# Kernel optimization log

Measured on AMD Instinct MI355X. Metric: run time of the kernel, lower is better.

## Reference

```python
import jax, jax.numpy as jnp
import numpy as np

B, S, T, H, E, V = 64, 128, 64, 512, 256, 10000


def setup_inputs() -> dict:
    key = jax.random.key(0)
    ks = jax.random.split(key, 16)
    w = 0.05
    return {
        "trg": jax.random.randint(ks[0], (B, T), 0, V),
        "encoder_hidden": jax.random.normal(ks[1], (B, S, 2 * H), jnp.float32),
        "src_lengths": jax.random.randint(ks[2], (B,), 1, S + 1),
        "h0": jax.random.normal(ks[3], (B, H), jnp.float32),
        "c0": jax.random.normal(ks[4], (B, H), jnp.float32),
        "emb_table": jax.random.normal(ks[5], (V, E), jnp.float32) * w,
        "Wkey": jax.random.normal(ks[6], (2 * H, H), jnp.float32) * w,      # attention.key_layer
        "Wquery": jax.random.normal(ks[7], (H, H), jnp.float32) * w,        # attention.query_layer
        "we": jax.random.normal(ks[8], (H,), jnp.float32) * w,              # attention.energy_layer
        "W_ih": jax.random.normal(ks[9], (4 * H, E + 2 * H), jnp.float32) * w,
        "W_hh": jax.random.normal(ks[10], (4 * H, H), jnp.float32) * w,
        "b_ih": jnp.zeros((4 * H,), jnp.float32),
        "b_hh": jnp.zeros((4 * H,), jnp.float32),
        "Wpre": jax.random.normal(ks[11], (3 * H + E, H), jnp.float32) * w,  # pre_output_layer (no bias)
        "Wgen": jax.random.normal(ks[12], (H, V), jnp.float32) * w,          # generator / softmax head
    }


def reference(trg, encoder_hidden, src_lengths, h0, c0, emb_table, Wkey, Wquery,
              we, W_ih, W_hh, b_ih, b_hh, Wpre, Wgen):
    # Teacher-forced unroll (teacher_forcing=True branch); dropout in eval mode.
    s = encoder_hidden.shape[1]
    proj_key = encoder_hidden @ Wkey                            # [B,S,H]
    mask = jnp.arange(s)[None, :] < src_lengths[:, None]        # [B,S]
    embs = emb_table[trg]                                       # [B,T,E]

    def step(carry, emb_t):
        h, c = carry                                            # [B,H] each
        q = h @ Wquery                                          # query = last-layer hidden
        e = jnp.einsum('bsh,h->bs', jnp.tanh(q[:, None, :] + proj_key), we)
        a = jax.nn.softmax(jnp.where(mask, e, -1e9), axis=-1)   # masked attention
        ctx = jnp.einsum('bs,bsd->bd', a, encoder_hidden)       # [B,2H]
        x = jnp.concatenate([emb_t, ctx], axis=-1)              # rnn_input
        g = x @ W_ih.T + h @ W_hh.T + b_ih + b_hh
        i_g, f_g, g_g, o_g = jnp.split(g, 4, axis=-1)           # torch LSTM gate order
        c_new = jax.nn.sigmoid(f_g) * c + jax.nn.sigmoid(i_g) * jnp.tanh(g_g)
        h_new = jax.nn.sigmoid(o_g) * jnp.tanh(c_new)
        pre = jnp.concatenate([emb_t, h_new, ctx], axis=-1) @ Wpre
        logp = jax.nn.log_softmax(pre @ Wgen, axis=-1)          # [B,V]
        return (h_new, c_new), logp

    (hf, cf), out = jax.lax.scan(step, (h0, c0), jnp.swapaxes(embs, 0, 1))
    return jnp.transpose(out, (1, 2, 0)), hf, cf                # out: [B,V,T]
```

## Files before the change

### kernel.cpp

```cpp
#include <hip/hip_runtime.h>

#define B 64
#define S 128
#define T 64
#define H 512
#define E 256
#define V 10000
#define H2 1024
#define G4 2048
#define KX 1536
#define KP 1792
#define VP 10112
#define NROW 4096

typedef unsigned short u16;
typedef __attribute__((ext_vector_type(8))) short bf16x8;
typedef __attribute__((ext_vector_type(4))) short bf16x4;
typedef __attribute__((ext_vector_type(4))) float floatx4;

__device__ inline float b2f(u16 h){
  union { unsigned int u; float f; } v; v.u = ((unsigned int)h) << 16; return v.f;
}
__device__ inline u16 f2b(float f){
  union { unsigned int u; float f; } v; v.f = f;
  unsigned int r = v.u + 0x7FFFu + ((v.u >> 16) & 1u);
  return (u16)(r >> 16);
}
__device__ inline float sigf(float x){ return 1.f/(1.f+__expf(-x)); }
__device__ inline float tanh_fast(float x){ float e=__expf(2.f*x); return 1.f - 2.f/(e+1.f); }

__device__ __forceinline__ void st_wt_u32(u16* p, unsigned v){
  asm volatile("global_store_dword %0, %1, off sc0 sc1" :: "v"(p), "v"(v) : "memory");
}
__device__ __forceinline__ void st_wt_u16(u16* p, unsigned v){
  asm volatile("global_store_short %0, %1, off sc0 sc1" :: "v"(p), "v"(v) : "memory");
}
__device__ __forceinline__ unsigned ld_if(unsigned* p){
  unsigned v;
  asm volatile("global_load_dword %0, %1, off sc0 sc1\ns_waitcnt vmcnt(0)" : "=v"(v) : "v"(p) : "memory");
  return v;
}
__device__ __forceinline__ void st_if(unsigned* p, unsigned v){
  asm volatile("global_store_dword %0, %1, off sc0 sc1\ns_waitcnt vmcnt(0)" :: "v"(p), "v"(v) : "memory");
}

#define BAR_WORDS (256*64)

__global__ void k_cast(const float* __restrict__ src, u16* __restrict__ dst, int n){
  int i = blockIdx.x*256 + threadIdx.x;
  if (i < n) dst[i] = f2b(src[i]);
}
__global__ void k_tct(const float* __restrict__ src, u16* __restrict__ dst, int R, int C){
  __shared__ float tile[64][65];
  int c0 = blockIdx.x*64, r0 = blockIdx.y*64;
  int tid = threadIdx.x;
  #pragma unroll
  for (int i=0;i<16;i++){
    int flat = i*256 + tid;
    int rr = flat >> 6, cc = flat & 63;
    int c = c0 + cc;
    tile[rr][cc] = (c < C) ? src[(size_t)(r0+rr)*C + c] : 0.f;
  }
  __syncthreads();
  #pragma unroll
  for (int i=0;i<16;i++){
    int flat = i*256 + tid;
    int cc = flat >> 6, rr = flat & 63;
    dst[(size_t)(c0+cc)*R + r0 + rr] = f2b(tile[rr][cc]);
  }
}
__global__ void k_wch(const float* __restrict__ wih, const float* __restrict__ whh, u16* __restrict__ o){
  int i = blockIdx.x*256 + threadIdx.x;
  if (i < G4*KX){
    int gp = i / KX, k = i % KX;
    int j = gp >> 2, gate = gp & 3, g = gate*H + j;
    float v = (k < H2) ? wih[(size_t)g*(E+H2) + E + k] : whh[(size_t)g*H + (k - H2)];
    o[i] = f2b(v);
  }
}
__global__ void k_wihe(const float* __restrict__ wih, u16* __restrict__ o){
  int i = blockIdx.x*256 + threadIdx.x;
  if (i < G4*E){
    int gp = i / E, e = i % E;
    int j = gp >> 2, gate = gp & 3, g = gate*H + j;
    o[i] = f2b(wih[(size_t)g*(E+H2) + e]);
  }
}
__global__ void k_bias(const float* __restrict__ bi, const float* __restrict__ bh, float* __restrict__ o){
  int i = blockIdx.x*256 + threadIdx.x;
  if (i < G4){
    int j = i >> 2, gate = i & 3, g = gate*H + j;
    o[i] = bi[g] + bh[g];
  }
}
__global__ void k_emb(const int* __restrict__ trg, const float* __restrict__ emb, u16* __restrict__ catp){
  int i = blockIdx.x*256 + threadIdx.x;
  if (i < NROW*E){
    int row = i >> 8, e = i & 255;
    int tok = trg[row];
    catp[(size_t)row*KP + e] = f2b(emb[(size_t)tok*E + e]);
  }
}
__global__ void k_init(const float* __restrict__ h0, u16* __restrict__ xgs){
  int i = blockIdx.x*256 + threadIdx.x;
  if (i < B*H){
    int b = i >> 9, j = i & 511;
    xgs[(size_t)b*KX + H2 + j] = f2b(h0[i]);
  }
}
__global__ void k_zero(unsigned* bar){
  int i = blockIdx.x*256 + threadIdx.x;
  if (i < BAR_WORDS) bar[i] = 0u;
}
__global__ void k_lse(const float* __restrict__ sep, float* __restrict__ lse){
  int r = blockIdx.x*256 + threadIdx.x;
  if (r < NROW){
    float s = 0.f;
    for (int i=0;i<79;i++) s += sep[(size_t)r*80 + i];
    lse[r] = logf(s);
  }
}

template<int TN, int EPI>
__global__ __launch_bounds__(256) void gemm_bf16(
    const u16* __restrict__ A, int lda,
    const u16* __restrict__ BT, int ldb,
    int K,
    u16* outb, int ldc,
    float* sep,
    float* outp, const float* lse)
{
  constexpr int NSUB = TN/16;
  constexpr int NB = TN/64;
  __shared__ u16 sA[64*32];
  __shared__ u16 sB[TN*32];
  __shared__ float Cx[(EPI==3) ? 128*65 : 1];
  __shared__ float lseb[(EPI==3)?64:1];

  const int tid = threadIdx.x;
  const int lane = tid & 63;
  const int wv = tid >> 6;
  const int row0 = blockIdx.x * 64;
  const int n0 = blockIdx.y * TN;

  floatx4 acc[NSUB];
  #pragma unroll
  for (int s=0;s<NSUB;s++) acc[s] = (floatx4){0.f,0.f,0.f,0.f};

  const int ar = tid >> 2;
  const int ch = tid & 3;
  const int swz = (ar >> 1) & 3;
  const int px = ((lane & 15) >> 1) & 3;

  const u16* gA = A + (size_t)(row0+ar)*lda + ch*8;
  bf16x8 pa = *(const bf16x8*)gA;
  bf16x8 pb[NB];
  #pragma unroll
  for (int i=0;i<NB;i++) pb[i] = *(const bf16x8*)(BT + (size_t)(n0+i*64+ar)*ldb + ch*8);

  for (int k0 = 0; k0 < K; k0 += 32){
    __syncthreads();
    *(bf16x8*)&sA[ar*32 + ((ch ^ swz)*8)] = pa;
    #pragma unroll
    for (int i=0;i<NB;i++)
      *(bf16x8*)&sB[(i*64+ar)*32 + ((ch ^ swz)*8)] = pb[i];
    __syncthreads();
    if (k0 + 32 < K){
      pa = *(const bf16x8*)(gA + k0 + 32);
      #pragma unroll
      for (int i=0;i<NB;i++) pb[i] = *(const bf16x8*)(BT + (size_t)(n0+i*64+ar)*ldb + k0+32 + ch*8);
    }
    bf16x8 af = *(const bf16x8*)&sA[(16*wv + (lane&15))*32 + (((lane>>4) ^ px)*8)];
    #pragma unroll
    for (int s=0;s<NSUB;s++){
      bf16x8 bfv = *(const bf16x8*)&sB[(16*s + (lane&15))*32 + (((lane>>4) ^ px)*8)];
      acc[s] = __builtin_amdgcn_mfma_f32_16x16x32_bf16(af, bfv, acc[s], 0, 0, 0);
    }
  }

  if constexpr (EPI == 0 || EPI == 4){
    #pragma unroll
    for (int s=0;s<NSUB;s++)
      #pragma unroll
      for (int r=0;r<4;r++){
        int row = row0 + 16*wv + ((lane>>4)<<2) + r;
        int col = n0 + 16*s + (lane&15);
        if (EPI == 4) row = ((row & 63) << 6) | (row >> 6);
        outb[(size_t)row*ldc + col] = f2b(acc[s][r]);
      }
  }
  if constexpr (EPI == 2){
    float sr[4] = {0.f,0.f,0.f,0.f};
    #pragma unroll
    for (int s=0;s<NSUB;s++){
      int col = n0 + 16*s + (lane&15);
      if (col < V){
        #pragma unroll
        for (int r=0;r<4;r++) sr[r] += __expf(acc[s][r]);
      }
    }
    #pragma unroll
    for (int r=0;r<4;r++){
      float v = sr[r];
      v += __shfl_xor(v,1); v += __shfl_xor(v,2); v += __shfl_xor(v,4); v += __shfl_xor(v,8);
      sr[r] = v;
    }
    if ((lane&15)==0){
      #pragma unroll
      for (int r=0;r<4;r++){
        int row = row0 + 16*wv + ((lane>>4)<<2) + r;
        sep[(size_t)row*80 + blockIdx.y] = sr[r];
      }
    }
  }
  if constexpr (EPI == 3){
    #pragma unroll
    for (int s=0;s<NSUB;s++)
      #pragma unroll
      for (int r=0;r<4;r++){
        int rl = 16*wv + ((lane>>4)<<2) + r;
        int cl = 16*s + (lane&15);
        Cx[cl*65 + rl] = acc[s][r];
      }
    if (tid < 64) lseb[tid] = lse[row0 + tid];
    __syncthreads();
    int b = blockIdx.x;
    for (int idx = tid; idx < TN*16; idx += 256){
      int vl = idx >> 4, q4 = idx & 15;
      int v = n0 + vl;
      if (v < V){
        floatx4 o;
        o[0] = Cx[vl*65 + q4*4+0] - lseb[q4*4+0];
        o[1] = Cx[vl*65 + q4*4+1] - lseb[q4*4+1];
        o[2] = Cx[vl*65 + q4*4+2] - lseb[q4*4+2];
        o[3] = Cx[vl*65 + q4*4+3] - lseb[q4*4+3];
        *(floatx4*)&outp[((size_t)b*V + v)*T + q4*4] = o;
      }
    }
  }
}

__device__ __forceinline__ void gbar(unsigned* bar, unsigned g){
  asm volatile("s_waitcnt vmcnt(0)" ::: "memory");
  __syncthreads();
  const int tid = threadIdx.x;
  if (blockIdx.x == 0){
    if (tid >= 1 && tid < 128){
      unsigned* a = bar + tid*64;
      int it = 0;
      while (ld_if(a) < g && ++it < 3000000) asm volatile("s_sleep 1":::);
    }
    __syncthreads();
    if (tid >= 1 && tid < 128) st_if(bar + (128+tid)*64, g);
  } else {
    if (tid == 0){
      st_if(bar + (unsigned)blockIdx.x*64, g);
      unsigned* r = bar + (128+(unsigned)blockIdx.x)*64;
      int it = 0;
      while (ld_if(r) < g && ++it < 3000000) asm volatile("s_sleep 1":::);
    }
  }
  __syncthreads();
}

__global__ __launch_bounds__(512) void decoder_loop(
    u16* __restrict__ xgs, const float* __restrict__ c0f, float* __restrict__ outp,
    const u16* __restrict__ pk, const u16* __restrict__ encb,
    const float* __restrict__ we, const int* __restrict__ lens,
    const u16* __restrict__ wqT, u16* __restrict__ cph,
    const u16* __restrict__ wch, const u16* __restrict__ gembt,
    const float* __restrict__ bias, unsigned* __restrict__ bar)
{
  __shared__ u16 sA[64*128];
  __shared__ u16 sB[32*128];
  __shared__ float Cx[64*36];
  __shared__ u16 hsb[H];
  __shared__ __align__(16) float qw[H];
  __shared__ __align__(16) float wel[H];
  __shared__ float ep[512];
  __shared__ float ev[S], al[S];
  __shared__ float smax, sinv;

  const int tid = threadIdx.x, lane = tid & 63, wv = tid >> 6;
  const int blk = blockIdx.x;
  const int xcd = blk & 7, slot = blk >> 3;

  if (slot < 8){
    const int b = xcd*8 + slot;
    const int lenb = lens[b];
    wel[tid] = we[tid];
    __syncthreads();

    for (int t=0; t<T; t++){
      u16* xgt = xgs + (size_t)t*B*KX;
      hsb[tid] = xgt[b*KX + H2 + tid];
      __syncthreads();
      {
        floatx4 accq[4];
        #pragma unroll
        for (int s=0;s<4;s++) accq[s] = (floatx4){0.f,0.f,0.f,0.f};
        const int kc = (lane>>4)*8;
        #pragma unroll 4
        for (int ks=0; ks<16; ks++){
          bf16x8 af = *(const bf16x8*)&hsb[ks*32 + kc];
          #pragma unroll
          for (int s=0;s<4;s++){
            const u16* bp = wqT + (size_t)(wv*64 + s*16 + (lane&15))*H + ks*32 + kc;
            accq[s] = __builtin_amdgcn_mfma_f32_16x16x32_bf16(af, *(const bf16x8*)bp, accq[s], 0, 0, 0);
          }
        }
        if (lane < 16){
          #pragma unroll
          for (int s=0;s<4;s++) qw[wv*64 + s*16 + lane] = accq[s][0];
        }
      }
      __syncthreads();
      {
        int s = tid >> 2, part = tid & 3;
        float a0 = 0.f;
        if (s < lenb){
          const u16* pr = pk + (size_t)(b*S + s)*H;
          #pragma unroll 4
          for (int m=0;m<16;m++){
            int k0 = part*8 + m*32;
            bf16x8 p8 = *(const bf16x8*)(pr + k0);
            floatx4 qa = *(const floatx4*)&qw[k0];
            floatx4 qb = *(const floatx4*)&qw[k0+4];
            floatx4 wa = *(const floatx4*)&wel[k0];
            floatx4 wb = *(const floatx4*)&wel[k0+4];
            #pragma unroll
            for (int i=0;i<4;i++){
              a0 += tanh_fast(qa[i] + b2f((u16)p8[i]))   * wa[i];
              a0 += tanh_fast(qb[i] + b2f((u16)p8[i+4])) * wb[i];
            }
          }
        }
        ep[tid] = a0;
      }
      __syncthreads();
      if (tid < S){
        float e = ep[tid*4] + ep[tid*4+1] + ep[tid*4+2] + ep[tid*4+3];
        ev[tid] = (tid < lenb) ? e : -1e30f;
      }
      __syncthreads();
      if (tid < 64){
        float m = fmaxf(ev[tid], ev[tid+64]);
        #pragma unroll
        for (int o=32;o>=1;o>>=1) m = fmaxf(m, __shfl_xor(m,o));
        if (tid==0) smax = m;
      }
      __syncthreads();
      if (tid < S) al[tid] = __expf(ev[tid]-smax);
      __syncthreads();
      if (tid < 64){
        float s2 = al[tid] + al[tid+64];
        #pragma unroll
        for (int o=32;o>=1;o>>=1) s2 += __shfl_xor(s2,o);
        if (tid==0) sinv = 1.f/s2;
      }
      __syncthreads();
      {
        float cx0=0.f, cx1=0.f;
        int d = tid*2;
        const u16* er = encb + (size_t)(b*S)*H2 + d;
        for (int ss=0; ss<lenb; ss++){
          unsigned int u = *(const unsigned int*)(er + (size_t)ss*H2);
          float a = al[ss];
          cx0 += a * b2f((u16)(u & 0xFFFFu));
          cx1 += a * b2f((u16)(u >> 16));
        }
        cx0 *= sinv; cx1 *= sinv;
        unsigned pack = ((unsigned)f2b(cx1) << 16) | (unsigned)f2b(cx0);
        st_wt_u32(xgt + (size_t)b*KX + d, pack);
        *(unsigned*)&cph[(size_t)(b*T + t)*KP + E + H + d] = pack;
      }
      gbar(bar, 2*t+1);
      gbar(bar, 2*t+2);
    }
  } else {
    const int g = slot - 8;
    const int n0 = xcd*256 + g*32;
    const int kh = wv >> 2, wr = wv & 3;
    const int rs0 = tid >> 4, gs = tid & 15;
    const int rowa = 16*wr + (lane & 15);
    const int pb_ = tid >> 3, jl = tid & 7;
    const int jglob = (n0 >> 2) + jl;
    float creg = c0f[pb_*H + jglob];
    floatx4 bias4 = *(const floatx4*)(bias + n0 + jl*4);

    for (int t=0; t<T; t++){
      gbar(bar, 2*t+1);
      const u16* xgt = xgs + (size_t)t*B*KX;
      u16* xgn = xgs + (size_t)(t+1)*B*KX;
      bf16x4 g4 = *(const bf16x4*)(gembt + (size_t)(t*B + pb_)*G4 + n0 + jl*4);

      floatx4 acc[2];
      acc[0] = (floatx4){0.f,0.f,0.f,0.f};
      acc[1] = (floatx4){0.f,0.f,0.f,0.f};
      bf16x8 a0 = *(const bf16x8*)(xgt + (size_t)rs0*KX + gs*8);
      bf16x8 a1 = *(const bf16x8*)(xgt + (size_t)(rs0+32)*KX + gs*8);
      bf16x8 b0 = *(const bf16x8*)(wch + (size_t)(n0+rs0)*KX + gs*8);

      for (int kk=0; kk<12; kk++){
        __syncthreads();
        *(bf16x8*)&sA[rs0*128 + ((gs ^ (rs0&7))*8)] = a0;
        *(bf16x8*)&sA[(rs0+32)*128 + ((gs ^ (rs0&7))*8)] = a1;
        *(bf16x8*)&sB[rs0*128 + ((gs ^ (rs0&7))*8)] = b0;
        __syncthreads();
        if (kk < 11){
          int ko = (kk+1)*128;
          a0 = *(const bf16x8*)(xgt + (size_t)rs0*KX + ko + gs*8);
          a1 = *(const bf16x8*)(xgt + (size_t)(rs0+32)*KX + ko + gs*8);
          b0 = *(const bf16x8*)(wch + (size_t)(n0+rs0)*KX + ko + gs*8);
        }
        #pragma unroll
        for (int ks=0; ks<2; ks++){
          int gq = kh*8 + ks*4 + (lane>>4);
          bf16x8 af = *(const bf16x8*)&sA[rowa*128 + ((gq ^ (rowa&7))*8)];
          #pragma unroll
          for (int s=0;s<2;s++){
            int rowb = 16*s + (lane & 15);
            bf16x8 bfv = *(const bf16x8*)&sB[rowb*128 + ((gq ^ (rowb&7))*8)];
            acc[s] = __builtin_amdgcn_mfma_f32_16x16x32_bf16(af, bfv, acc[s], 0, 0, 0);
          }
        }
      }
      {
        int r0 = 16*wr + ((lane>>4)<<2);
        if (kh == 1){
          #pragma unroll
          for (int s=0;s<2;s++)
            #pragma unroll
            for (int r=0;r<4;r++) Cx[(r0+r)*36 + 16*s + (lane&15)] = acc[s][r];
        }
      }
      __syncthreads();
      {
        int r0 = 16*wr + ((lane>>4)<<2);
        if (kh == 0){
          #pragma unroll
          for (int s=0;s<2;s++)
            #pragma unroll
            for (int r=0;r<4;r++) Cx[(r0+r)*36 + 16*s + (lane&15)] += acc[s][r];
        }
      }
      __syncthreads();
      {
        float gi = Cx[pb_*36 + jl*4+0] + b2f((u16)g4[0]) + bias4[0];
        float gf = Cx[pb_*36 + jl*4+1] + b2f((u16)g4[1]) + bias4[1];
        float gg = Cx[pb_*36 + jl*4+2] + b2f((u16)g4[2]) + bias4[2];
        float go = Cx[pb_*36 + jl*4+3] + b2f((u16)g4[3]) + bias4[3];
        float cn = sigf(gf)*creg + sigf(gi)*tanhf(gg);
        float hn = sigf(go)*tanhf(cn);
        creg = cn;
        u16 hb = f2b(hn);
        st_wt_u16(xgn + (size_t)pb_*KX + H2 + jglob, (unsigned)hb);
        cph[(size_t)(pb_*T + t)*KP + E + jglob] = hb;
        if (t == T-1){
          outp[(size_t)B*V*T + pb_*H + jglob] = hn;
          outp[(size_t)B*V*T + B*H + pb_*H + jglob] = cn;
        }
      }
      gbar(bar, 2*t+2);
    }
  }
}

static inline int cdiv(int a, int b){ return (a + b - 1) / b; }

extern "C" void kernel_launch(void* const* d_in, const int* in_sizes, int n_in,
                              void* d_out, int out_size, void* d_ws, size_t ws_size,
                              hipStream_t stream)
{
  (void)in_sizes; (void)n_in; (void)out_size; (void)ws_size;
  const int*   trg  = (const int*)d_in[0];
  const float* enc  = (const float*)d_in[1];
  const int*   lens = (const int*)d_in[2];
  const float* h0   = (const float*)d_in[3];
  const float* c0   = (const float*)d_in[4];
  const float* embt = (const float*)d_in[5];
  const float* wkey = (const float*)d_in[6];
  const float* wqry = (const float*)d_in[7];
  const float* we   = (const float*)d_in[8];
  const float* wih  = (const float*)d_in[9];
  const float* whh  = (const float*)d_in[10];
  const float* bi   = (const float*)d_in[11];
  const float* bh   = (const float*)d_in[12];
  const float* wpre = (const float*)d_in[13];
  const float* wgen = (const float*)d_in[14];
  float* out = (float*)d_out;

  char* p = (char*)d_ws;
  auto carve = [&](size_t bytes)->char*{ char* r = p; p += (bytes + 255) & ~(size_t)255; return r; };
  u16*   encb  = (u16*)  carve((size_t)B*S*H2*2);
  u16*   pkb   = (u16*)  carve((size_t)B*S*H*2);
  u16*   catp  = (u16*)  carve((size_t)NROW*KP*2);
  u16*   gembb = (u16*)  carve((size_t)NROW*G4*2);
  u16*   preb  = (u16*)  carve((size_t)NROW*H*2);
  u16*   wgt   = (u16*)  carve((size_t)VP*H*2);
  u16*   wch   = (u16*)  carve((size_t)G4*KX*2);
  u16*   wihe  = (u16*)  carve((size_t)G4*E*2);
  u16*   wkeyT = (u16*)  carve((size_t)H*H2*2);
  u16*   wqT   = (u16*)  carve((size_t)H*H*2);
  u16*   wpreT = (u16*)  carve((size_t)H*KP*2);
  u16*   xgs   = (u16*)  carve((size_t)(T+1)*B*KX*2);
  float* biasp = (float*)carve((size_t)G4*4);
  float* sep   = (float*)carve((size_t)NROW*80*4);
  float* lse   = (float*)carve((size_t)NROW*4);
  unsigned* bar = (unsigned*)carve(BAR_WORDS*4);

  k_cast<<<cdiv(B*S*H2,256),256,0,stream>>>(enc, encb, B*S*H2);
  k_tct<<<dim3(H/64, H/64),256,0,stream>>>(wqry, wqT, H, H);
  k_tct<<<dim3(H/64, H2/64),256,0,stream>>>(wkey, wkeyT, H2, H);
  k_tct<<<dim3(H/64, KP/64),256,0,stream>>>(wpre, wpreT, KP, H);
  k_tct<<<dim3(VP/64, H/64),256,0,stream>>>(wgen, wgt, H, V);
  k_wch<<<cdiv(G4*KX,256),256,0,stream>>>(wih, whh, wch);
  k_wihe<<<cdiv(G4*E,256),256,0,stream>>>(wih, wihe);
  k_bias<<<cdiv(G4,256),256,0,stream>>>(bi, bh, biasp);
  k_emb<<<cdiv(NROW*E,256),256,0,stream>>>(trg, embt, catp);
  k_init<<<cdiv(B*H,256),256,0,stream>>>(h0, xgs);
  k_zero<<<cdiv(BAR_WORDS,256),256,0,stream>>>(bar);

  gemm_bf16<64,0><<<dim3(B*S/64, H/64),256,0,stream>>>(
      encb, H2, wkeyT, H2, H2, pkb, H, nullptr, nullptr, nullptr);
  gemm_bf16<64,4><<<dim3(NROW/64, G4/64),256,0,stream>>>(
      catp, KP, wihe, E, E, gembb, G4, nullptr, nullptr, nullptr);

  decoder_loop<<<128,512,0,stream>>>(xgs, c0, out, pkb, encb, we, lens,
                                     wqT, catp, wch, gembb, biasp, bar);

  gemm_bf16<64,0><<<dim3(NROW/64, H/64),256,0,stream>>>(
      catp, KP, wpreT, KP, KP, preb, H, nullptr, nullptr, nullptr);

  gemm_bf16<128,2><<<dim3(NROW/64, VP/128),256,0,stream>>>(
      preb, H, wgt, H, H, nullptr, 0, sep, nullptr, nullptr);
  k_lse<<<cdiv(NROW,256),256,0,stream>>>(sep, lse);
  gemm_bf16<128,3><<<dim3(NROW/64, VP/128),256,0,stream>>>(
      preb, H, wgt, H, H, nullptr, 0, nullptr, out, lse);
}
```

Measured before the change: 2.953 ms.

## Replace centralized grid barriers with producer/consumer flag waits between attention and LSTM blocks

Swaps the two-phase centralized grid barrier, where block 0 gathers arrivals and then broadcasts a release, for per-role flags. Attention blocks publish a ctx-ready flag per batch row and wait only on the 64 LSTM-block h flags. LSTM blocks publish an h-ready flag and wait only on the 64 ctx flags. This removes the extra hop through block 0 and one of the two barriers per step. It also swaps divisions for hardware reciprocal in the sigmoid, tanh and softmax normalizer, at a small cost in accuracy.

```diff
diff --git a/kernel.cpp b/kernel.cpp
--- a/kernel.cpp
+++ b/kernel.cpp
@@ -26,8 +26,9 @@
   unsigned int r = v.u + 0x7FFFu + ((v.u >> 16) & 1u);
   return (u16)(r >> 16);
 }
-__device__ inline float sigf(float x){ return 1.f/(1.f+__expf(-x)); }
-__device__ inline float tanh_fast(float x){ float e=__expf(2.f*x); return 1.f - 2.f/(e+1.f); }
+__device__ __forceinline__ float rcpf(float x){ return __builtin_amdgcn_rcpf(x); }
+__device__ inline float sigf(float x){ return rcpf(1.f + __expf(-x)); }
+__device__ inline float tanh_fast(float x){ float e=__expf(2.f*x); return 1.f - 2.f*rcpf(e+1.f); }
 
 __device__ __forceinline__ void st_wt_u32(u16* p, unsigned v){
   asm volatile("global_store_dword %0, %1, off sc0 sc1" :: "v"(p), "v"(v) : "memory");
@@ -44,7 +45,7 @@
   asm volatile("global_store_dword %0, %1, off sc0 sc1\ns_waitcnt vmcnt(0)" :: "v"(p), "v"(v) : "memory");
 }
 
-#define BAR_WORDS (256*64)
+#define BAR_WORDS (128*64)
 
 __global__ void k_cast(const float* __restrict__ src, u16* __restrict__ dst, int n){
   int i = blockIdx.x*256 + threadIdx.x;
@@ -240,25 +241,11 @@
   }
 }
 
-__device__ __forceinline__ void gbar(unsigned* bar, unsigned g){
-  asm volatile("s_waitcnt vmcnt(0)" ::: "memory");
-  __syncthreads();
-  const int tid = threadIdx.x;
-  if (blockIdx.x == 0){
-    if (tid >= 1 && tid < 128){
-      unsigned* a = bar + tid*64;
-      int it = 0;
-      while (ld_if(a) < g && ++it < 3000000) asm volatile("s_sleep 1":::);
-    }
-    __syncthreads();
-    if (tid >= 1 && tid < 128) st_if(bar + (128+tid)*64, g);
-  } else {
-    if (tid == 0){
-      st_if(bar + (unsigned)blockIdx.x*64, g);
-      unsigned* r = bar + (128+(unsigned)blockIdx.x)*64;
-      int it = 0;
-      while (ld_if(r) < g && ++it < 3000000) asm volatile("s_sleep 1":::);
-    }
+__device__ __forceinline__ void wait_flags(unsigned* base, unsigned g){
+  if (threadIdx.x < 64){
+    unsigned* p = base + (unsigned)threadIdx.x*64;
+    int it = 0;
+    while (ld_if(p) < g && ++it < 5000000) asm volatile("s_sleep 1":::);
   }
   __syncthreads();
 }
@@ -284,6 +271,8 @@
   const int tid = threadIdx.x, lane = tid & 63, wv = tid >> 6;
   const int blk = blockIdx.x;
   const int xcd = blk & 7, slot = blk >> 3;
+  unsigned* flag_ctx = bar;
+  unsigned* flag_h   = bar + 64*64;
 
   if (slot < 8){
     const int b = xcd*8 + slot;
@@ -292,6 +281,7 @@
     __syncthreads();
 
     for (int t=0; t<T; t++){
+      wait_flags(flag_h, (unsigned)t);
       u16* xgt = xgs + (size_t)t*B*KX;
       hsb[tid] = xgt[b*KX + H2 + tid];
       __syncthreads();
@@ -356,7 +346,7 @@
         float s2 = al[tid] + al[tid+64];
         #pragma unroll
         for (int o=32;o>=1;o>>=1) s2 += __shfl_xor(s2,o);
-        if (tid==0) sinv = 1.f/s2;
+        if (tid==0) sinv = rcpf(s2);
       }
       __syncthreads();
       {
@@ -374,11 +364,14 @@
         st_wt_u32(xgt + (size_t)b*KX + d, pack);
         *(unsigned*)&cph[(size_t)(b*T + t)*KP + E + H + d] = pack;
       }
-      gbar(bar, 2*t+1);
-      gbar(bar, 2*t+2);
+      asm volatile("s_waitcnt vmcnt(0)" ::: "memory");
+      __syncthreads();
+      if (tid == 0) st_if(flag_ctx + (unsigned)b*64, (unsigned)(t+1));
+      __syncthreads();
     }
   } else {
     const int g = slot - 8;
+    const int gid = xcd*8 + g;
     const int n0 = xcd*256 + g*32;
     const int kh = wv >> 2, wr = wv & 3;
     const int rs0 = tid >> 4, gs = tid & 15;
@@ -389,7 +382,7 @@
     floatx4 bias4 = *(const floatx4*)(bias + n0 + jl*4);
 
     for (int t=0; t<T; t++){
-      gbar(bar, 2*t+1);
+      wait_flags(flag_ctx, (unsigned)(t+1));
       const u16* xgt = xgs + (size_t)t*B*KX;
       u16* xgn = xgs + (size_t)(t+1)*B*KX;
       bf16x4 g4 = *(const bf16x4*)(gembt + (size_t)(t*B + pb_)*G4 + n0 + jl*4);
@@ -461,7 +454,10 @@
           outp[(size_t)B*V*T + B*H + pb_*H + jglob] = cn;
         }
       }
-      gbar(bar, 2*t+2);
+      asm volatile("s_waitcnt vmcnt(0)" ::: "memory");
+      __syncthreads();
+      if (tid == 0) st_if(flag_h + (unsigned)gid*64, (unsigned)(t+1));
+      __syncthreads();
     }
   }
 }
```

New measurement: 2.501 ms (median of 2 runs). 1.18x faster.
